# Kernel tuning notes

Measured on AMD Instinct MI355X. Metric: run time of the kernel, lower is better.

Reference implementation:

```python
import jax, jax.numpy as jnp
import numpy as np

THRESHOLD = 1.0  # snntorch Leaky default threshold
BETA = 0.9
ATAN_ALPHA = 2.0  # snntorch surrogate.atan default alpha

# Heaviside forward with ATan surrogate gradient (snntorch surrogate.atan)
@jax.custom_vjp
def atan_spike(x):
    return (x > 0).astype(x.dtype)

def _atan_fwd(x):
    return atan_spike(x), x

def _atan_bwd(x, g):
    # d/dx ~ (alpha/2) / (1 + (pi/2 * alpha * x)^2)
    return (g * (ATAN_ALPHA / 2.0) / (1.0 + (jnp.pi / 2.0 * ATAN_ALPHA * x) ** 2),)

atan_spike.defvjp(_atan_fwd, _atan_bwd)


def setup_inputs() -> dict:
    key = jax.random.key(0)
    kx, kw = jax.random.split(key)
    T, B, N_in, N_out = 128, 64, 1024, 1024
    x = (jax.random.uniform(kx, (T, B, N_in)) < 0.2).astype(jnp.float32)
    # kaiming_uniform_(mode='fan_in', nonlinearity='tanh'): gain=5/3, bound=gain*sqrt(3/fan_in)
    bound = (5.0 / 3.0) * np.sqrt(3.0 / N_in)
    W = jax.random.uniform(kw, (N_out, N_in), minval=-bound, maxval=bound, dtype=jnp.float32)
    return {"x": x, "W": W}


def reference(x, W):
    # x: (T, B, N_in) -> current: (T, B, N_out) via bias-free linear (vmapped over T)
    cur = jnp.einsum('tbi,oi->tbo', x, W)
    mem0 = jnp.zeros(cur.shape[1:], cur.dtype)

    # snntorch Leaky (reset_mechanism='subtract'):
    #   reset_t = detached spike of previous mem; mem_t = beta*mem_{t-1} + I_t - reset_t*thr
    #   spk_t = fire(mem_t)
    def step(mem, c_t):
        reset = jax.lax.stop_gradient(atan_spike(mem - THRESHOLD))
        mem_new = BETA * mem + c_t - reset * THRESHOLD
        spk = atan_spike(mem_new - THRESHOLD)
        return mem_new, (spk, mem_new)

    _, (spk_rec, mem_rec) = jax.lax.scan(step, mem0, cur)
    return spk_rec, mem_rec
```

## Files before the change

kernel.cpp:

```cpp
#include <hip/hip_runtime.h>
#include <cstddef>

constexpr int T_STEPS = 128;
constexpr int BATCH   = 64;
constexpr int N_IN    = 1024;
constexpr int N_OUT   = 1024;
constexpr int M_TOTAL = T_STEPS * BATCH;
constexpr int NEURONS = BATCH * N_OUT;
constexpr int OUT_HALF = T_STEPS * NEURONS;

constexpr double W_SCALE     = 17179869184.0;
constexpr double W_INV_SCALE = 1.0 / 17179869184.0;

typedef int i32x4 __attribute__((ext_vector_type(4)));

__global__ __launch_bounds__(256)
void prep_all(const float* __restrict__ x, const float* __restrict__ W,
              signed char* __restrict__ xi8, signed char* __restrict__ pi8)
{
    const int bid = blockIdx.x;
    if (bid < 2048) {
        const int i = bid * 256 + threadIdx.x;
        const float4 a = ((const float4*)x)[4 * i + 0];
        const float4 b = ((const float4*)x)[4 * i + 1];
        const float4 c = ((const float4*)x)[4 * i + 2];
        const float4 d = ((const float4*)x)[4 * i + 3];
        const float f[16] = {a.x,a.y,a.z,a.w, b.x,b.y,b.z,b.w,
                             c.x,c.y,c.z,c.w, d.x,d.y,d.z,d.w};
        union { signed char b[16]; int4 v; } u;
#pragma unroll
        for (int j = 0; j < 16; ++j) u.b[j] = (signed char)(f[j] != 0.0f);
        ((int4*)xi8)[i] = u.v;
    } else {
        const int i = (bid - 2048) * 256 + threadIdx.x;
        const float4 wv = ((const float4*)W)[i];
        const float wf[4] = {wv.x, wv.y, wv.z, wv.w};
        union { signed char b[4]; unsigned u; } dig[4];
#pragma unroll
        for (int j = 0; j < 4; ++j) {
            int q = __double2int_rn((double)wf[j] * W_SCALE);
            const int d0 = ((q + 128) & 255) - 128;  q = (q - d0) >> 8;
            const int d1 = ((q + 128) & 255) - 128;  q = (q - d1) >> 8;
            const int d2 = ((q + 128) & 255) - 128;  q = (q - d2) >> 8;
            dig[0].b[j] = (signed char)d0;
            dig[1].b[j] = (signed char)d1;
            dig[2].b[j] = (signed char)d2;
            dig[3].b[j] = (signed char)q;
        }
        unsigned* pw = (unsigned*)pi8;
#pragma unroll
        for (int p = 0; p < 4; ++p) pw[p * 262144 + i] = dig[p].u;
    }
}

__device__ __forceinline__ void gload_lds16(const signed char* g, signed char* l)
{
    __builtin_amdgcn_global_load_lds(
        (const __attribute__((address_space(1))) unsigned*)(g),
        (__attribute__((address_space(3))) unsigned*)(l), 16, 0, 0);
}

__global__ __launch_bounds__(512)
void gemm_lif(const signed char* __restrict__ xi8, const signed char* __restrict__ pi8,
              unsigned* __restrict__ outw)
{
    __shared__ __align__(16) unsigned char smem[128 * 66 * 8];
    signed char* As = (signed char*)smem;
    signed char* Bs = (signed char*)smem + 8192;
    double (*curL)[66] = (double (*)[66])smem;

    const int tid  = threadIdx.x;
    const int b    = blockIdx.y;
    const int o0   = blockIdx.x * 64;
    const int lane = tid & 63;
    const int w    = tid >> 6;
    const int wm   = w >> 2;
    const int wn   = w & 3;
    const int l15  = lane & 15;
    const int kg   = lane >> 4;
    const int swzr = (l15 >> 1) & 3;

    const int srow   = lane >> 2;
    const int schunk = (lane & 3) ^ ((lane >> 3) & 3);

    i32x4 acc[4][4] = {};

    for (int k0 = 0; k0 < N_IN; k0 += 64) {
        gload_lds16(xi8 + (size_t)((w * 16 + srow) * 64 + b) * N_IN + k0 + schunk * 16,
                    As + w * 1024);
#pragma unroll
        for (int i = 0; i < 2; ++i) {
            const int seg  = w * 2 + i;
            const int p    = seg >> 2;
            const int rowp = (seg & 3) * 16 + srow;
            gload_lds16(pi8 + (size_t)p * 1048576 + (size_t)(o0 + rowp) * N_IN
                            + k0 + schunk * 16,
                        Bs + seg * 1024);
        }
        __syncthreads();

        i32x4 af[4], bf[4];
#pragma unroll
        for (int fm = 0; fm < 4; ++fm) {
            const int row = wm * 64 + fm * 16 + l15;
            af[fm] = *(const i32x4*)(As + row * 64 + (kg ^ swzr) * 16);
        }
        {
            const int row = wn * 16 + l15;
#pragma unroll
            for (int p = 0; p < 4; ++p)
                bf[p] = *(const i32x4*)(Bs + p * 4096 + row * 64 + (kg ^ swzr) * 16);
        }

#pragma unroll
        for (int p = 0; p < 4; ++p)
#pragma unroll
            for (int fm = 0; fm < 4; ++fm)
                acc[p][fm] = __builtin_amdgcn_mfma_i32_16x16x64_i8(
                    af[fm], bf[p], acc[p][fm], 0, 0, 0);
        __syncthreads();
    }

    const int onl = wn * 16 + l15;
#pragma unroll
    for (int fm = 0; fm < 4; ++fm)
#pragma unroll
        for (int r = 0; r < 4; ++r) {
            const int t = wm * 64 + fm * 16 + kg * 4 + r;
            const double q = (double)acc[3][fm][r] * 16777216.0
                           + (double)acc[2][fm][r] * 65536.0
                           + (double)acc[1][fm][r] * 256.0
                           + (double)acc[0][fm][r];
            curL[t][onl] = q * W_INV_SCALE;
        }
    __syncthreads();

    if (tid < 64) {
        const int oc = tid;
        const size_t nbase = (size_t)b * N_OUT + o0 + oc;
        double mem = 0.0;
        double c[8], cn[8];
#pragma unroll
        for (int j = 0; j < 8; ++j) c[j] = curL[j][oc];
        for (int t0 = 0; t0 < T_STEPS; t0 += 8) {
            if (t0 + 8 < T_STEPS) {
#pragma unroll
                for (int j = 0; j < 8; ++j) cn[j] = curL[t0 + 8 + j][oc];
            }
#pragma unroll
            for (int j = 0; j < 8; ++j) {
                const double reset = (mem > 1.0) ? 1.0 : 0.0;
                mem = 0.9 * mem + c[j] - reset;
                const size_t idx = (size_t)(t0 + j) * NEURONS + nbase;
                outw[idx]            = (mem > 1.0) ? 0x3f800000u : 0u;
                outw[OUT_HALF + idx] = __float_as_uint((float)mem);
            }
#pragma unroll
            for (int j = 0; j < 8; ++j) c[j] = cn[j];
        }
    }
}

extern "C" void kernel_launch(void* const* d_in, const int* in_sizes, int n_in,
                              void* d_out, int out_size, void* d_ws, size_t ws_size,
                              hipStream_t stream)
{
    const float* x = (const float*)d_in[0];
    const float* W = (const float*)d_in[1];
    unsigned* outw = (unsigned*)d_out;

    signed char* xi8 = (signed char*)d_ws;
    signed char* pi8 = xi8 + (size_t)M_TOTAL * N_IN;

    prep_all<<<3072, 256, 0, stream>>>(x, W, xi8, pi8);

    dim3 ggrid(N_OUT / 64, BATCH);
    gemm_lif<<<ggrid, 512, 0, stream>>>(xi8, pi8, outw);
}
```

Before: 132.4 us.

## Triple-buffer GEMM k-loop with async LDS loads and raised MFMA priority

Replaces the single-buffered load/sync/compute k-loop with a three-stage LDS ring that issues global_load_lds two tiles ahead, waiting on vmcnt counters so loads overlap MFMA work. It also raises wave priority around the MFMA block with s_setprio. Shared memory grows to three 24 KB buffers, which may lower occupancy. The manual vmcnt counts and the raw s_barrier without an LDS wait rely on exact load counts to stay correct.

```diff
diff --git a/kernel.cpp b/kernel.cpp
--- a/kernel.cpp
+++ b/kernel.cpp
@@ -60,13 +60,14 @@
         (__attribute__((address_space(3))) unsigned*)(l), 16, 0, 0);
 }
 
+constexpr int BUF_BYTES = 24576;
+constexpr int NT_K      = 16;
+
 __global__ __launch_bounds__(512)
 void gemm_lif(const signed char* __restrict__ xi8, const signed char* __restrict__ pi8,
               unsigned* __restrict__ outw)
 {
-    __shared__ __align__(16) unsigned char smem[128 * 66 * 8];
-    signed char* As = (signed char*)smem;
-    signed char* Bs = (signed char*)smem + 8192;
+    __shared__ __align__(16) unsigned char smem[3 * BUF_BYTES];
     double (*curL)[66] = (double (*)[66])smem;
 
     const int tid  = threadIdx.x;
@@ -85,19 +86,42 @@
 
     i32x4 acc[4][4] = {};
 
-    for (int k0 = 0; k0 < N_IN; k0 += 64) {
-        gload_lds16(xi8 + (size_t)((w * 16 + srow) * 64 + b) * N_IN + k0 + schunk * 16,
-                    As + w * 1024);
-#pragma unroll
-        for (int i = 0; i < 2; ++i) {
-            const int seg  = w * 2 + i;
-            const int p    = seg >> 2;
-            const int rowp = (seg & 3) * 16 + srow;
-            gload_lds16(pi8 + (size_t)p * 1048576 + (size_t)(o0 + rowp) * N_IN
-                            + k0 + schunk * 16,
-                        Bs + seg * 1024);
-        }
-        __syncthreads();
+    const signed char* gA = xi8 + (size_t)((w * 16 + srow) * 64 + b) * N_IN + schunk * 16;
+
+#define STAGE(KT, BUF)                                                          \
+    {                                                                           \
+        signed char* As_ = (signed char*)smem + (BUF) * BUF_BYTES;              \
+        signed char* Bs_ = As_ + 8192;                                          \
+        const int k0_ = (KT) * 64;                                              \
+        gload_lds16(gA + k0_, As_ + w * 1024);                                  \
+        _Pragma("unroll")                                                       \
+        for (int i_ = 0; i_ < 2; ++i_) {                                        \
+            const int seg_  = w * 2 + i_;                                       \
+            const int p_    = seg_ >> 2;                                        \
+            const int rowp_ = (seg_ & 3) * 16 + srow;                           \
+            gload_lds16(pi8 + (size_t)p_ * 1048576                              \
+                            + (size_t)(o0 + rowp_) * N_IN + k0_ + schunk * 16,  \
+                        Bs_ + seg_ * 1024);                                     \
+        }                                                                       \
+    }
+
+    STAGE(0, 0);
+    STAGE(1, 1);
+
+    for (int kt = 0; kt < NT_K; ++kt) {
+        const int bufc = kt % 3;
+        if (kt < NT_K - 2) {
+            STAGE(kt + 2, (kt + 2) % 3);
+            asm volatile("s_waitcnt vmcnt(6)" ::: "memory");
+        } else if (kt == NT_K - 2) {
+            asm volatile("s_waitcnt vmcnt(3)" ::: "memory");
+        } else {
+            asm volatile("s_waitcnt vmcnt(0)" ::: "memory");
+        }
+        __builtin_amdgcn_s_barrier();
+
+        const signed char* As = (const signed char*)smem + bufc * BUF_BYTES;
+        const signed char* Bs = As + 8192;
 
         i32x4 af[4], bf[4];
 #pragma unroll
@@ -112,14 +136,18 @@
                 bf[p] = *(const i32x4*)(Bs + p * 4096 + row * 64 + (kg ^ swzr) * 16);
         }
 
+        __builtin_amdgcn_s_setprio(1);
 #pragma unroll
         for (int p = 0; p < 4; ++p)
 #pragma unroll
             for (int fm = 0; fm < 4; ++fm)
                 acc[p][fm] = __builtin_amdgcn_mfma_i32_16x16x64_i8(
                     af[fm], bf[p], acc[p][fm], 0, 0, 0);
-        __syncthreads();
-    }
+        __builtin_amdgcn_s_setprio(0);
+
+        __builtin_amdgcn_s_barrier();
+    }
+#undef STAGE
 
     const int onl = wn * 16 + l15;
 #pragma unroll
```

After: 129.5 us. 1.02x faster.
